# Kernel tuning notes

Measured on AMD Instinct MI355X. Metric: run time of the kernel, lower is better.

## Reference

```python
import jax, jax.numpy as jnp
import numpy as np

N, E, G = 50000, 800000, 512
EMB, HID, NSHAPE, NCOLOR, NCLS = 128, 256, 64, 64, 32


def setup_inputs() -> dict:
    key = jax.random.key(0)
    ks = jax.random.split(key, 12)
    s = 0.05
    return {
        "x": jax.random.randint(ks[0], (N, 2), 0, NSHAPE),
        "edge_index": jax.random.randint(ks[1], (2, E), 0, N),
        "batch": jnp.sort(jax.random.randint(ks[2], (N,), 0, G)),
        "shape_emb": jax.random.normal(ks[3], (NSHAPE, EMB)) * s,
        "color_emb": jax.random.normal(ks[4], (NCOLOR, EMB)) * s,
        # SAGEConv: lin_l (applied to aggregated neighbors, with bias), lin_r (root, no bias)
        "w1l": jax.random.normal(ks[5], (HID, 2 * EMB)) * s,
        "b1l": jnp.zeros((HID,)),
        "w1r": jax.random.normal(ks[6], (HID, 2 * EMB)) * s,
        "w2l": jax.random.normal(ks[7], (HID, HID)) * s,
        "b2l": jnp.zeros((HID,)),
        "w2r": jax.random.normal(ks[8], (HID, HID)) * s,
        "wc": jax.random.normal(ks[9], (NCLS, HID)) * s,
        "bc": jnp.zeros((NCLS,)),
    }


def _sage_conv(h, src, dst, wl, bl, wr):
    # mean-aggregate messages h[src] onto dst, then lin_l(aggr) + lin_r(h)
    msg = h[src]  # [E, d]
    agg = jax.ops.segment_sum(msg, dst, num_segments=N)  # [N, d]
    deg = jax.ops.segment_sum(jnp.ones((src.shape[0],), h.dtype), dst, num_segments=N)
    agg = agg / jnp.maximum(deg, 1.0)[:, None]
    return agg @ wl.T + bl + h @ wr.T


def reference(x, edge_index, batch, shape_emb, color_emb,
              w1l, b1l, w1r, w2l, b2l, w2r, wc, bc):
    src, dst = edge_index[0], edge_index[1]
    h = jnp.concatenate([shape_emb[x[:, 0]], color_emb[x[:, 1]]], axis=-1)  # [N, 2*EMB]
    h = jax.nn.relu(_sage_conv(h, src, dst, w1l, b1l, w1r))
    h = jax.nn.relu(_sage_conv(h, src, dst, w2l, b2l, w2r))
    # global mean pool over graphs
    hs = jax.ops.segment_sum(h, batch, num_segments=G)  # [G, HID]
    cnt = jax.ops.segment_sum(jnp.ones((N,), h.dtype), batch, num_segments=G)
    hg = hs / jnp.maximum(cnt, 1.0)[:, None]
    return hg @ wc.T + bc  # [G, NCLS]
```

## Files before the change

### kernel.cpp

```cpp
#include <hip/hip_runtime.h>
#include <hip/hip_bf16.h>


#define EMB   128
#define HID   256
#define NCLS  32
#define DIM   256

typedef __attribute__((ext_vector_type(8))) short short8v;
typedef __attribute__((ext_vector_type(4))) float float4v;

__device__ __forceinline__ unsigned short f2bf(float f) {
    unsigned int u = __float_as_uint(f);
    unsigned int r = u + 0x7FFFu + ((u >> 16) & 1u);
    return (unsigned short)(r >> 16);
}
__device__ __forceinline__ float bf2f(unsigned short s) {
    return __uint_as_float(((unsigned int)s) << 16);
}

__global__ void build_bq2(const float* __restrict__ w1l, const float* __restrict__ w1r,
                          const float* __restrict__ w2l, const float* __restrict__ w2r,
                          unsigned short* __restrict__ b1hi, unsigned short* __restrict__ b1lo,
                          unsigned short* __restrict__ b2hi, unsigned short* __restrict__ b2lo) {
    int tid = blockIdx.x * 256 + threadIdx.x;
    int which = tid >> 17;
    int r = tid & 0x1FFFF;
    int k = r >> 8, o = r & 255;
    const float* wl = which ? w2l : w1l;
    const float* wr = which ? w2r : w1r;
    float v = (k < 256) ? wl[o * 256 + k] : wr[o * 256 + (k - 256)];
    unsigned short h = f2bf(v);
    unsigned short l = f2bf(v - bf2f(h));
    int idx = (((k >> 3) * 256) + o) * 8 + (k & 7);
    (which ? b2hi : b1hi)[idx] = h;
    (which ? b2lo : b1lo)[idx] = l;
}

__global__ void embed_bf16(const int* __restrict__ x,
                           const float* __restrict__ se, const float* __restrict__ ce,
                           unsigned short* __restrict__ hb, int n_nodes) {
    int tid = blockIdx.x * 256 + threadIdx.x;
    if (tid >= n_nodes * 32) return;
    int n = tid >> 5, c = tid & 31;
    const float* src = (c < 16) ? (se + (size_t)x[n * 2] * EMB + c * 8)
                                : (ce + (size_t)x[n * 2 + 1] * EMB + (c - 16) * 8);
    float4 v0 = *(const float4*)src;
    float4 v1 = *(const float4*)(src + 4);
    ushort4 o0 = make_ushort4(f2bf(v0.x), f2bf(v0.y), f2bf(v0.z), f2bf(v0.w));
    ushort4 o1 = make_ushort4(f2bf(v1.x), f2bf(v1.y), f2bf(v1.z), f2bf(v1.w));
    *(ushort4*)(hb + (size_t)tid * 8)     = o0;
    *(ushort4*)(hb + (size_t)tid * 8 + 4) = o1;
}


__global__ void count_deg(const int* __restrict__ dst, int* __restrict__ deg, int E) {
    int e = blockIdx.x * 256 + threadIdx.x;
    if (e < E) atomicAdd(&deg[dst[e]], 1);
}

__global__ void scan_block(const int* __restrict__ deg, int* __restrict__ rowptr,
                           int* __restrict__ bsums, int n) {
    __shared__ int s[256];
    int t = threadIdx.x;
    int i = blockIdx.x * 256 + t;
    int v = (i < n) ? deg[i] : 0;
    s[t] = v; __syncthreads();
    for (int off = 1; off < 256; off <<= 1) {
        int x = (t >= off) ? s[t - off] : 0;
        __syncthreads(); s[t] += x; __syncthreads();
    }
    if (i < n) rowptr[i] = s[t] - v;
    if (t == 255) bsums[blockIdx.x] = s[255];
}

__global__ void scan_sums(int* __restrict__ bsums, int nb, int* __restrict__ rowptr,
                          int n, int E) {
    __shared__ int s[256];
    int t = threadIdx.x;
    int v = (t < nb) ? bsums[t] : 0;
    s[t] = v; __syncthreads();
    for (int off = 1; off < 256; off <<= 1) {
        int x = (t >= off) ? s[t - off] : 0;
        __syncthreads(); s[t] += x; __syncthreads();
    }
    if (t < nb) bsums[t] = s[t] - v;
    if (t == 0) rowptr[n] = E;
}

__global__ void scan_add(int* __restrict__ rowptr, const int* __restrict__ bsums, int n) {
    int i = blockIdx.x * 256 + threadIdx.x;
    if (i < n) rowptr[i] += bsums[i >> 8];
}

__global__ void fill_csr(const int* __restrict__ src, const int* __restrict__ dst,
                         const int* __restrict__ rowptr, int* __restrict__ cursor,
                         int* __restrict__ csr, int E) {
    int e = blockIdx.x * 256 + threadIdx.x;
    if (e >= E) return;
    int d = dst[e];
    int pos = rowptr[d] + atomicAdd(&cursor[d], 1);
    csr[pos] = src[e];
}

__global__ void aggregate_bf16(const unsigned short* __restrict__ hb,
                               const int* __restrict__ rowptr, const int* __restrict__ csr,
                               unsigned short* __restrict__ ahi, unsigned short* __restrict__ alo,
                               int n_nodes) {
    int wid = (blockIdx.x * 256 + threadIdx.x) >> 6;
    int lane = threadIdx.x & 63;
    if (wid >= n_nodes) return;
    int beg = rowptr[wid], end = rowptr[wid + 1];
    float a0 = 0.f, a1 = 0.f, a2 = 0.f, a3 = 0.f;
    int k = beg;
    for (; k + 3 < end; k += 4) {
        int s0 = csr[k], s1 = csr[k + 1], s2 = csr[k + 2], s3 = csr[k + 3];
        ushort4 u0 = *(const ushort4*)(hb + (size_t)s0 * DIM + lane * 4);
        ushort4 u1 = *(const ushort4*)(hb + (size_t)s1 * DIM + lane * 4);
        ushort4 u2 = *(const ushort4*)(hb + (size_t)s2 * DIM + lane * 4);
        ushort4 u3 = *(const ushort4*)(hb + (size_t)s3 * DIM + lane * 4);
        a0 += bf2f(u0.x) + bf2f(u1.x) + bf2f(u2.x) + bf2f(u3.x);
        a1 += bf2f(u0.y) + bf2f(u1.y) + bf2f(u2.y) + bf2f(u3.y);
        a2 += bf2f(u0.z) + bf2f(u1.z) + bf2f(u2.z) + bf2f(u3.z);
        a3 += bf2f(u0.w) + bf2f(u1.w) + bf2f(u2.w) + bf2f(u3.w);
    }
    for (; k < end; ++k) {
        ushort4 u = *(const ushort4*)(hb + (size_t)csr[k] * DIM + lane * 4);
        a0 += bf2f(u.x); a1 += bf2f(u.y); a2 += bf2f(u.z); a3 += bf2f(u.w);
    }
    int d = end - beg;
    float inv = 1.0f / (float)(d > 1 ? d : 1);
    float v[4] = {a0 * inv, a1 * inv, a2 * inv, a3 * inv};
    unsigned short hs[4], ls[4];
#pragma unroll
    for (int i = 0; i < 4; ++i) {
        hs[i] = f2bf(v[i]);
        ls[i] = f2bf(v[i] - bf2f(hs[i]));
    }
    *(ushort4*)(ahi + (size_t)wid * DIM + lane * 4) = make_ushort4(hs[0], hs[1], hs[2], hs[3]);
    *(ushort4*)(alo + (size_t)wid * DIM + lane * 4) = make_ushort4(ls[0], ls[1], ls[2], ls[3]);
}

__global__ void __launch_bounds__(256)
gemm_mfma(const unsigned short* __restrict__ Ahi, const unsigned short* __restrict__ Alo,
          const unsigned short* __restrict__ Hinb,
          const unsigned short* __restrict__ Bhi, const unsigned short* __restrict__ Blo,
          const float* __restrict__ bias,
          float* __restrict__ Houtf, unsigned short* __restrict__ Houtb, int M) {
    const int t = threadIdx.x;
    const int w = t >> 6, lane = t & 63;
    const int lrow = lane & 15, koct = lane >> 4;
    const int nw = w * 64;
    const int m0 = blockIdx.x * 64;

    size_t arow[4];
#pragma unroll
    for (int mt = 0; mt < 4; ++mt) {
        int r = m0 + mt * 16 + lrow;
        arow[mt] = (size_t)(r < M ? r : M - 1) * DIM;
    }

    float4v acc[4][4];
#pragma unroll
    for (int i = 0; i < 4; ++i)
#pragma unroll
        for (int j = 0; j < 4; ++j) acc[i][j] = (float4v){0.f, 0.f, 0.f, 0.f};

#pragma unroll 2
    for (int kt = 0; kt < 8; ++kt) {
        const int kofs = kt * 32 + koct * 8;
        const int kg = kt * 4 + koct;
        short8v ah[4], al[4], bh[4], bl[4];
#pragma unroll
        for (int mt = 0; mt < 4; ++mt) {
            ah[mt] = *(const short8v*)(Ahi + arow[mt] + kofs);
            al[mt] = *(const short8v*)(Alo + arow[mt] + kofs);
        }
#pragma unroll
        for (int nt = 0; nt < 4; ++nt) {
            size_t bofs = ((size_t)kg * 256 + (nw + nt * 16 + lrow)) * 8;
            bh[nt] = *(const short8v*)(Bhi + bofs);
            bl[nt] = *(const short8v*)(Blo + bofs);
        }
#pragma unroll
        for (int mt = 0; mt < 4; ++mt)
#pragma unroll
            for (int nt = 0; nt < 4; ++nt) {
                acc[mt][nt] = __builtin_amdgcn_mfma_f32_16x16x32_bf16(ah[mt], bh[nt], acc[mt][nt], 0, 0, 0);
                acc[mt][nt] = __builtin_amdgcn_mfma_f32_16x16x32_bf16(ah[mt], bl[nt], acc[mt][nt], 0, 0, 0);
                acc[mt][nt] = __builtin_amdgcn_mfma_f32_16x16x32_bf16(al[mt], bh[nt], acc[mt][nt], 0, 0, 0);
            }
    }

#pragma unroll 2
    for (int kt = 0; kt < 8; ++kt) {
        const int kofs = kt * 32 + koct * 8;
        const int kg = (kt + 8) * 4 + koct;
        short8v ah[4], bh[4], bl[4];
#pragma unroll
        for (int mt = 0; mt < 4; ++mt)
            ah[mt] = *(const short8v*)(Hinb + arow[mt] + kofs);
#pragma unroll
        for (int nt = 0; nt < 4; ++nt) {
            size_t bofs = ((size_t)kg * 256 + (nw + nt * 16 + lrow)) * 8;
            bh[nt] = *(const short8v*)(Bhi + bofs);
            bl[nt] = *(const short8v*)(Blo + bofs);
        }
#pragma unroll
        for (int mt = 0; mt < 4; ++mt)
#pragma unroll
            for (int nt = 0; nt < 4; ++nt) {
                acc[mt][nt] = __builtin_amdgcn_mfma_f32_16x16x32_bf16(ah[mt], bh[nt], acc[mt][nt], 0, 0, 0);
                acc[mt][nt] = __builtin_amdgcn_mfma_f32_16x16x32_bf16(ah[mt], bl[nt], acc[mt][nt], 0, 0, 0);
            }
    }

    float bv[4];
#pragma unroll
    for (int nt = 0; nt < 4; ++nt) bv[nt] = bias[nw + nt * 16 + lrow];

#pragma unroll
    for (int mt = 0; mt < 4; ++mt) {
#pragma unroll
        for (int r = 0; r < 4; ++r) {
            int grow = m0 + mt * 16 + koct * 4 + r;
            if (grow >= M) continue;
#pragma unroll
            for (int nt = 0; nt < 4; ++nt) {
                float vv = fmaxf(acc[mt][nt][r] + bv[nt], 0.f);
                int col = nw + nt * 16 + lrow;
                if (Houtf) Houtf[(size_t)grow * DIM + col] = vv;
                if (Houtb) Houtb[(size_t)grow * DIM + col] = f2bf(vv);
            }
        }
    }
}


__global__ void pool_kernel(const float* __restrict__ h, const int* __restrict__ batch,
                            float* __restrict__ hg, int n_nodes) {
    int g = blockIdx.x;
    int t = threadIdx.x;
    int lo = 0, hi = n_nodes;
    while (lo < hi) { int mid = (lo + hi) >> 1; if (batch[mid] < g) lo = mid + 1; else hi = mid; }
    int start = lo;
    hi = n_nodes;
    while (lo < hi) { int mid = (lo + hi) >> 1; if (batch[mid] < g + 1) lo = mid + 1; else hi = mid; }
    int end = lo;
    float acc = 0.f;
    for (int n = start; n < end; ++n) acc += h[(size_t)n * DIM + t];
    int c = end - start;
    hg[g * DIM + t] = acc / (float)(c > 1 ? c : 1);
}

__global__ void head_kernel(const float* __restrict__ hg, const float* __restrict__ wc,
                            const float* __restrict__ bc, float* __restrict__ out, int total) {
    int tid = blockIdx.x * 256 + threadIdx.x;
    if (tid >= total) return;
    int g = tid >> 5, c = tid & 31;
    const float* hr = hg + (size_t)g * DIM;
    const float* wr = wc + (size_t)c * DIM;
    float acc = bc[c];
    for (int k = 0; k < DIM; ++k) acc = fmaf(hr[k], wr[k], acc);
    out[tid] = acc;
}


extern "C" void kernel_launch(void* const* d_in, const int* in_sizes, int n_in,
                              void* d_out, int out_size, void* d_ws, size_t ws_size,
                              hipStream_t stream) {
    const int* x      = (const int*)d_in[0];
    const int* ei     = (const int*)d_in[1];
    const int* batch  = (const int*)d_in[2];
    const float* se   = (const float*)d_in[3];
    const float* ce   = (const float*)d_in[4];
    const float* w1l  = (const float*)d_in[5];
    const float* b1l  = (const float*)d_in[6];
    const float* w1r  = (const float*)d_in[7];
    const float* w2l  = (const float*)d_in[8];
    const float* b2l  = (const float*)d_in[9];
    const float* w2r  = (const float*)d_in[10];
    const float* wc   = (const float*)d_in[11];
    const float* bc   = (const float*)d_in[12];
    float* out = (float*)d_out;

    const int N = in_sizes[0] / 2;
    const int E = in_sizes[1] / 2;
    const int G = out_size / NCLS;
    const int* src = ei;
    const int* dst = ei + E;

    float* h2 = (float*)d_ws;
    unsigned short* agghi = (unsigned short*)(h2 + (size_t)N * DIM);
    unsigned short* agglo = agghi + (size_t)N * DIM;
    unsigned short* h0b   = agglo + (size_t)N * DIM;
    unsigned short* h1b   = h0b + (size_t)N * DIM;
    unsigned short* B1hi  = h1b + (size_t)N * DIM;
    unsigned short* B1lo  = B1hi + 131072;
    unsigned short* B2hi  = B1lo + 131072;
    unsigned short* B2lo  = B2hi + 131072;
    float* hg  = (float*)(B2lo + 131072);
    int* deg    = (int*)(hg + (size_t)G * DIM);
    int* rowptr = deg + N;
    int* cursor = rowptr + (N + 1);
    int* csr    = cursor + N;
    int* bsums  = csr + E;

    hipMemsetAsync(deg, 0, (size_t)(3 * N + 1) * sizeof(int), stream);

    embed_bf16<<<(N * 32 + 255) / 256, 256, 0, stream>>>(x, se, ce, h0b, N);

    int eblocks = (E + 255) / 256;
    count_deg<<<eblocks, 256, 0, stream>>>(dst, deg, E);
    int sblocks = (N + 255) / 256;
    scan_block<<<sblocks, 256, 0, stream>>>(deg, rowptr, bsums, N);
    scan_sums<<<1, 256, 0, stream>>>(bsums, sblocks, rowptr, N, E);
    scan_add<<<sblocks, 256, 0, stream>>>(rowptr, bsums, N);
    fill_csr<<<eblocks, 256, 0, stream>>>(src, dst, rowptr, cursor, csr, E);

    build_bq2<<<1024, 256, 0, stream>>>(w1l, w1r, w2l, w2r, B1hi, B1lo, B2hi, B2lo);

    int gblocks = (N + 63) / 64;
    int ablocks = (N * 64 + 255) / 256;

    aggregate_bf16<<<ablocks, 256, 0, stream>>>(h0b, rowptr, csr, agghi, agglo, N);
    gemm_mfma<<<gblocks, 256, 0, stream>>>(agghi, agglo, h0b, B1hi, B1lo, b1l, nullptr, h1b, N);

    aggregate_bf16<<<ablocks, 256, 0, stream>>>(h1b, rowptr, csr, agghi, agglo, N);
    gemm_mfma<<<gblocks, 256, 0, stream>>>(agghi, agglo, h1b, B2hi, B2lo, b2l, h2, nullptr, N);

    pool_kernel<<<G, 256, 0, stream>>>(h2, batch, hg, N);
    head_kernel<<<(G * NCLS + 255) / 256, 256, 0, stream>>>(hg, wc, bc, out, G * NCLS);
}
```

Measured before the change: 495.9 us.

## Store GEMM A-operands in MFMA fragment layout and retile GEMM into 128x64 blocks

Aggregation outputs and node features are now also written in a blocked layout: groups of 16 rows by 8 k-values, so each lane's 8-element MFMA A fragment is contiguous across the wave. The aim is more coalesced A loads in the GEMM. The GEMM moves to a 2D grid of 128-row by 64-column tiles with a 2x2 wave arrangement and a launch bound of 3 blocks per CU, which halves the per-wave B fragments and accumulators. The cost is extra feature-matrix copies, scattered 2-byte writes of the fragment-layout output, and each A tile being read by four column blocks instead of once.

```diff
diff --git a/kernel.cpp b/kernel.cpp
--- a/kernel.cpp
+++ b/kernel.cpp
@@ -39,7 +39,8 @@
 
 __global__ void embed_bf16(const int* __restrict__ x,
                            const float* __restrict__ se, const float* __restrict__ ce,
-                           unsigned short* __restrict__ hb, int n_nodes) {
+                           unsigned short* __restrict__ hb, unsigned short* __restrict__ hf,
+                           int n_nodes) {
     int tid = blockIdx.x * 256 + threadIdx.x;
     if (tid >= n_nodes * 32) return;
     int n = tid >> 5, c = tid & 31;
@@ -51,6 +52,9 @@
     ushort4 o1 = make_ushort4(f2bf(v1.x), f2bf(v1.y), f2bf(v1.z), f2bf(v1.w));
     *(ushort4*)(hb + (size_t)tid * 8)     = o0;
     *(ushort4*)(hb + (size_t)tid * 8 + 4) = o1;
+    size_t fo = ((size_t)(n >> 4) * 32 + c) * 128 + (n & 15) * 8;
+    *(ushort4*)(hf + fo)     = o0;
+    *(ushort4*)(hf + fo + 4) = o1;
 }
 
 
@@ -105,7 +109,7 @@
 
 __global__ void aggregate_bf16(const unsigned short* __restrict__ hb,
                                const int* __restrict__ rowptr, const int* __restrict__ csr,
-                               unsigned short* __restrict__ ahi, unsigned short* __restrict__ alo,
+                               unsigned short* __restrict__ ahiF, unsigned short* __restrict__ aloF,
                                int n_nodes) {
     int wid = (blockIdx.x * 256 + threadIdx.x) >> 6;
     int lane = threadIdx.x & 63;
@@ -137,55 +141,61 @@
         hs[i] = f2bf(v[i]);
         ls[i] = f2bf(v[i] - bf2f(hs[i]));
     }
-    *(ushort4*)(ahi + (size_t)wid * DIM + lane * 4) = make_ushort4(hs[0], hs[1], hs[2], hs[3]);
-    *(ushort4*)(alo + (size_t)wid * DIM + lane * 4) = make_ushort4(ls[0], ls[1], ls[2], ls[3]);
-}
-
-__global__ void __launch_bounds__(256)
+    size_t base = ((size_t)(wid >> 4) * 32 + (lane >> 1)) * 128 + (wid & 15) * 8 + (lane & 1) * 4;
+    *(ushort4*)(ahiF + base) = make_ushort4(hs[0], hs[1], hs[2], hs[3]);
+    *(ushort4*)(aloF + base) = make_ushort4(ls[0], ls[1], ls[2], ls[3]);
+}
+
+__global__ void __launch_bounds__(256, 3)
 gemm_mfma(const unsigned short* __restrict__ Ahi, const unsigned short* __restrict__ Alo,
-          const unsigned short* __restrict__ Hinb,
+          const unsigned short* __restrict__ Hf,
           const unsigned short* __restrict__ Bhi, const unsigned short* __restrict__ Blo,
           const float* __restrict__ bias,
-          float* __restrict__ Houtf, unsigned short* __restrict__ Houtb, int M) {
+          float* __restrict__ Houtf, unsigned short* __restrict__ Houtb,
+          unsigned short* __restrict__ Hfrag, int M) {
     const int t = threadIdx.x;
     const int w = t >> 6, lane = t & 63;
     const int lrow = lane & 15, koct = lane >> 4;
-    const int nw = w * 64;
-    const int m0 = blockIdx.x * 64;
-
-    size_t arow[4];
+    const int wm = w >> 1, wn = w & 1;
+    const int rb = blockIdx.y * 128 + wm * 64;
+    const int cb = blockIdx.x * 64 + wn * 32;
+    const int mbmax = (M >> 4) - 1;
+
+    size_t abase[4];
 #pragma unroll
     for (int mt = 0; mt < 4; ++mt) {
-        int r = m0 + mt * 16 + lrow;
-        arow[mt] = (size_t)(r < M ? r : M - 1) * DIM;
-    }
-
-    float4v acc[4][4];
+        int mb = (rb >> 4) + mt;
+        if (mb > mbmax) mb = mbmax;
+        abase[mt] = (size_t)mb * 32 * 128 + lrow * 8;
+    }
+    const int col0 = cb + lrow;
+
+    float4v acc[4][2];
 #pragma unroll
     for (int i = 0; i < 4; ++i)
 #pragma unroll
-        for (int j = 0; j < 4; ++j) acc[i][j] = (float4v){0.f, 0.f, 0.f, 0.f};
+        for (int j = 0; j < 2; ++j) acc[i][j] = (float4v){0.f, 0.f, 0.f, 0.f};
 
 #pragma unroll 2
     for (int kt = 0; kt < 8; ++kt) {
-        const int kofs = kt * 32 + koct * 8;
+        const size_t kof = (size_t)(kt * 4 + koct) * 128;
         const int kg = kt * 4 + koct;
-        short8v ah[4], al[4], bh[4], bl[4];
+        short8v ah[4], al[4], bh[2], bl[2];
 #pragma unroll
         for (int mt = 0; mt < 4; ++mt) {
-            ah[mt] = *(const short8v*)(Ahi + arow[mt] + kofs);
-            al[mt] = *(const short8v*)(Alo + arow[mt] + kofs);
+            ah[mt] = *(const short8v*)(Ahi + abase[mt] + kof);
+            al[mt] = *(const short8v*)(Alo + abase[mt] + kof);
         }
 #pragma unroll
-        for (int nt = 0; nt < 4; ++nt) {
-            size_t bofs = ((size_t)kg * 256 + (nw + nt * 16 + lrow)) * 8;
+        for (int nt = 0; nt < 2; ++nt) {
+            size_t bofs = ((size_t)kg * 256 + col0 + nt * 16) * 8;
             bh[nt] = *(const short8v*)(Bhi + bofs);
             bl[nt] = *(const short8v*)(Blo + bofs);
         }
 #pragma unroll
         for (int mt = 0; mt < 4; ++mt)
 #pragma unroll
-            for (int nt = 0; nt < 4; ++nt) {
+            for (int nt = 0; nt < 2; ++nt) {
                 acc[mt][nt] = __builtin_amdgcn_mfma_f32_16x16x32_bf16(ah[mt], bh[nt], acc[mt][nt], 0, 0, 0);
                 acc[mt][nt] = __builtin_amdgcn_mfma_f32_16x16x32_bf16(ah[mt], bl[nt], acc[mt][nt], 0, 0, 0);
                 acc[mt][nt] = __builtin_amdgcn_mfma_f32_16x16x32_bf16(al[mt], bh[nt], acc[mt][nt], 0, 0, 0);
@@ -194,43 +204,45 @@
 
 #pragma unroll 2
     for (int kt = 0; kt < 8; ++kt) {
-        const int kofs = kt * 32 + koct * 8;
+        const size_t kof = (size_t)(kt * 4 + koct) * 128;
         const int kg = (kt + 8) * 4 + koct;
-        short8v ah[4], bh[4], bl[4];
+        short8v ah[4], bh[2], bl[2];
 #pragma unroll
         for (int mt = 0; mt < 4; ++mt)
-            ah[mt] = *(const short8v*)(Hinb + arow[mt] + kofs);
-#pragma unroll
-        for (int nt = 0; nt < 4; ++nt) {
-            size_t bofs = ((size_t)kg * 256 + (nw + nt * 16 + lrow)) * 8;
+            ah[mt] = *(const short8v*)(Hf + abase[mt] + kof);
+#pragma unroll
+        for (int nt = 0; nt < 2; ++nt) {
+            size_t bofs = ((size_t)kg * 256 + col0 + nt * 16) * 8;
             bh[nt] = *(const short8v*)(Bhi + bofs);
             bl[nt] = *(const short8v*)(Blo + bofs);
         }
 #pragma unroll
         for (int mt = 0; mt < 4; ++mt)
 #pragma unroll
-            for (int nt = 0; nt < 4; ++nt) {
+            for (int nt = 0; nt < 2; ++nt) {
                 acc[mt][nt] = __builtin_amdgcn_mfma_f32_16x16x32_bf16(ah[mt], bh[nt], acc[mt][nt], 0, 0, 0);
                 acc[mt][nt] = __builtin_amdgcn_mfma_f32_16x16x32_bf16(ah[mt], bl[nt], acc[mt][nt], 0, 0, 0);
             }
     }
 
-    float bv[4];
-#pragma unroll
-    for (int nt = 0; nt < 4; ++nt) bv[nt] = bias[nw + nt * 16 + lrow];
+    float bv[2];
+#pragma unroll
+    for (int nt = 0; nt < 2; ++nt) bv[nt] = bias[cb + nt * 16 + lrow];
 
 #pragma unroll
     for (int mt = 0; mt < 4; ++mt) {
 #pragma unroll
         for (int r = 0; r < 4; ++r) {
-            int grow = m0 + mt * 16 + koct * 4 + r;
+            int grow = rb + mt * 16 + koct * 4 + r;
             if (grow >= M) continue;
-#pragma unroll
-            for (int nt = 0; nt < 4; ++nt) {
+            size_t fbase = ((size_t)(grow >> 4) * 32) * 128 + (grow & 15) * 8;
+#pragma unroll
+            for (int nt = 0; nt < 2; ++nt) {
                 float vv = fmaxf(acc[mt][nt][r] + bv[nt], 0.f);
-                int col = nw + nt * 16 + lrow;
+                int col = cb + nt * 16 + lrow;
                 if (Houtf) Houtf[(size_t)grow * DIM + col] = vv;
                 if (Houtb) Houtb[(size_t)grow * DIM + col] = f2bf(vv);
+                if (Hfrag) Hfrag[fbase + (size_t)(col >> 3) * 128 + (col & 7)] = f2bf(vv);
             }
         }
     }
@@ -291,14 +303,16 @@
     const int* dst = ei + E;
 
     float* h2 = (float*)d_ws;
-    unsigned short* agghi = (unsigned short*)(h2 + (size_t)N * DIM);
-    unsigned short* agglo = agghi + (size_t)N * DIM;
-    unsigned short* h0b   = agglo + (size_t)N * DIM;
-    unsigned short* h1b   = h0b + (size_t)N * DIM;
-    unsigned short* B1hi  = h1b + (size_t)N * DIM;
-    unsigned short* B1lo  = B1hi + 131072;
-    unsigned short* B2hi  = B1lo + 131072;
-    unsigned short* B2lo  = B2hi + 131072;
+    unsigned short* agghiF = (unsigned short*)(h2 + (size_t)N * DIM);
+    unsigned short* aggloF = agghiF + (size_t)N * DIM;
+    unsigned short* h0b    = aggloF + (size_t)N * DIM;
+    unsigned short* h0f    = h0b + (size_t)N * DIM;
+    unsigned short* h1b    = h0f + (size_t)N * DIM;
+    unsigned short* h1f    = h1b + (size_t)N * DIM;
+    unsigned short* B1hi   = h1f + (size_t)N * DIM;
+    unsigned short* B1lo   = B1hi + 131072;
+    unsigned short* B2hi   = B1lo + 131072;
+    unsigned short* B2lo   = B2hi + 131072;
     float* hg  = (float*)(B2lo + 131072);
     int* deg    = (int*)(hg + (size_t)G * DIM);
     int* rowptr = deg + N;
@@ -308,7 +322,7 @@
 
     hipMemsetAsync(deg, 0, (size_t)(3 * N + 1) * sizeof(int), stream);
 
-    embed_bf16<<<(N * 32 + 255) / 256, 256, 0, stream>>>(x, se, ce, h0b, N);
+    embed_bf16<<<(N * 32 + 255) / 256, 256, 0, stream>>>(x, se, ce, h0b, h0f, N);
 
     int eblocks = (E + 255) / 256;
     count_deg<<<eblocks, 256, 0, stream>>>(dst, deg, E);
@@ -320,14 +334,16 @@
 
     build_bq2<<<1024, 256, 0, stream>>>(w1l, w1r, w2l, w2r, B1hi, B1lo, B2hi, B2lo);
 
-    int gblocks = (N + 63) / 64;
+    dim3 ggrid(256 / 64, (N + 127) / 128);
     int ablocks = (N * 64 + 255) / 256;
 
-    aggregate_bf16<<<ablocks, 256, 0, stream>>>(h0b, rowptr, csr, agghi, agglo, N);
-    gemm_mfma<<<gblocks, 256, 0, stream>>>(agghi, agglo, h0b, B1hi, B1lo, b1l, nullptr, h1b, N);
-
-    aggregate_bf16<<<ablocks, 256, 0, stream>>>(h1b, rowptr, csr, agghi, agglo, N);
-    gemm_mfma<<<gblocks, 256, 0, stream>>>(agghi, agglo, h1b, B2hi, B2lo, b2l, h2, nullptr, N);
+    aggregate_bf16<<<ablocks, 256, 0, stream>>>(h0b, rowptr, csr, agghiF, aggloF, N);
+    gemm_mfma<<<ggrid, 256, 0, stream>>>(agghiF, aggloF, h0f, B1hi, B1lo, b1l,
+                                         nullptr, h1b, h1f, N);
+
+    aggregate_bf16<<<ablocks, 256, 0, stream>>>(h1b, rowptr, csr, agghiF, aggloF, N);
+    gemm_mfma<<<ggrid, 256, 0, stream>>>(agghiF, aggloF, h1f, B2hi, B2lo, b2l,
+                                         h2, nullptr, nullptr, N);
 
     pool_kernel<<<G, 256, 0, stream>>>(h2, batch, hg, N);
     head_kernel<<<(G * NCLS + 255) / 256, 256, 0, stream>>>(hg, wc, bc, out, G * NCLS);
```

New measurement: 536.4 us. 8.1% more time.
